# Performance work log

Measured on AMD Instinct MI355X. Metric: run time of the kernel, lower is better.

Reference implementation:

```python
import jax, jax.numpy as jnp
import numpy as np

NEG_INF = jnp.float32(-1e30)  # stand-in for -inf; relu(-inf) == relu(-1e30) == 0


def setup_inputs() -> dict:
    key = jax.random.key(0)
    ks = jax.random.split(key, 8)
    B, S, E = 4, 4096, 512
    query = jax.random.normal(ks[0], (B, S, E), dtype=jnp.float32)
    k_in = jax.random.normal(ks[1], (B, S, E), dtype=jnp.float32)
    v_in = jax.random.normal(ks[2], (B, S, E), dtype=jnp.float32)
    mask = jax.random.randint(ks[3], (B, S, S), 0, 2) > 0  # bool [B,S,S]
    scale = 1.0 / np.sqrt(E)
    W1 = jax.random.uniform(ks[4], (E, E), jnp.float32, -scale, scale)
    b1 = jax.random.uniform(ks[5], (E,), jnp.float32, -scale, scale)
    W2 = jax.random.uniform(ks[6], (E, E), jnp.float32, -scale, scale)
    b2 = jax.random.uniform(ks[7], (E,), jnp.float32, -scale, scale)
    return {"query": query, "key": k_in, "value": v_in, "mask": mask,
            "W1": W1, "b1": b1, "W2": W2, "b2": b2}


def reference(query, key, value, mask, W1, b1, W2, b2):
    # key projection: nn.Linear -> x @ W.T + b
    k = jnp.einsum('bse,fe->bsf', key, W1) + b1
    # raw dot-product correlation scores [B, S, S]
    scores = jnp.einsum('bqe,bke->bqk', query, k)
    # module forces mask[:, :, 0] = True, then fills ~mask with -inf
    m = mask.at[:, :, 0].set(True)
    scores = jnp.where(m, scores, NEG_INF)
    # ReLU instead of softmax (no normalization); dropout is identity in eval
    alpha = jax.nn.relu(scores)
    # value projection then AV matmul
    v = jnp.einsum('bse,fe->bsf', value, W2) + b2
    out = jnp.einsum('bqk,bke->bqe', alpha, v)
    return out
```

## Files before the change

kernel.cpp:

```cpp
#include <hip/hip_runtime.h>
#include <cstdint>


typedef __bf16 bf16x8 __attribute__((ext_vector_type(8)));
typedef float f32x4 __attribute__((ext_vector_type(4)));

__device__ __forceinline__ unsigned short f2bf(float f) {
  unsigned int u = __float_as_uint(f);
  u += 0x7fffu + ((u >> 16) & 1u);
  return (unsigned short)(u >> 16);
}

__device__ __forceinline__ void async_load16(const void* g, void* l) {
  __builtin_amdgcn_global_load_lds(
      (const __attribute__((address_space(1))) unsigned int*)(uintptr_t)g,
      (__attribute__((address_space(3))) unsigned int*)(unsigned int)(uintptr_t)l,
      16, 0, 0);
}

__global__ void __launch_bounds__(256)
prep(const float* __restrict__ q, const float* __restrict__ k,
     const float* __restrict__ v, const float* __restrict__ w1,
     const float* __restrict__ w2, const int* __restrict__ m,
     unsigned short* __restrict__ qb, unsigned short* __restrict__ kb,
     unsigned short* __restrict__ vb, unsigned short* __restrict__ w1b,
     unsigned short* __restrict__ w2b, unsigned int* __restrict__ bits) {
  const int b = blockIdx.x, tid = threadIdx.x;
  if (b < 24576) {
    const int which = b >> 13;
    const int idx = (b & 8191) * 256 + tid;
    const float* in = (which == 0) ? q : (which == 1) ? k : v;
    unsigned short* out = (which == 0) ? qb : (which == 1) ? kb : vb;
    float4 f = ((const float4*)in)[idx];
    ushort4 o;
    o.x = f2bf(f.x); o.y = f2bf(f.y); o.z = f2bf(f.z); o.w = f2bf(f.w);
    ((ushort4*)out)[idx] = o;
  } else if (b < 25088) {
    const int which = (b - 24576) >> 8;
    const int idx = ((b - 24576) & 255) * 256 + tid;
    const float* in = (which == 0) ? w1 : w2;
    unsigned short* out = (which == 0) ? w1b : w2b;
    float4 f = ((const float4*)in)[idx];
    ushort4 o;
    o.x = f2bf(f.x); o.y = f2bf(f.y); o.z = f2bf(f.z); o.w = f2bf(f.w);
    ((ushort4*)out)[idx] = o;
  } else {
    const int lane = tid & 63;
    const size_t wid = (size_t)(b - 25088) * 4 + (tid >> 6);
    const size_t base = wid * 256;
    unsigned long long bl[4];
#pragma unroll
    for (int c = 0; c < 4; ++c) {
      size_t e = base + (size_t)c * 64 + lane;
      int col = (int)(e & 4095);
      bl[c] = __ballot((m[e] != 0) || (col == 0));
    }
    if (lane < 8)
      bits[base / 32 + lane] = (unsigned int)(bl[lane >> 1] >> ((lane & 1) * 32));
  }
}

__global__ void __launch_bounds__(256)
proj(const unsigned short* __restrict__ Kb, const unsigned short* __restrict__ W1b,
     unsigned short* __restrict__ Kp, const float* __restrict__ b1,
     const unsigned short* __restrict__ W2b, const unsigned short* __restrict__ Vb,
     unsigned short* __restrict__ Vpt, const float* __restrict__ b2) {
  constexpr int K = 512;
  constexpr long long SE = 4096LL * 512;
  __shared__ unsigned short sA[2 * 128 * 32];
  __shared__ unsigned short sB[2 * 128 * 32];

  const int L = blockIdx.x;
  const unsigned short *Ab, *Bb;
  unsigned short* C;
  const float* bias;
  int tm0, tn0, N, epi;
  if (L < 512) {
    tn0 = (L & 3) * 128; tm0 = (L >> 2) * 128;
    Ab = Kb; Bb = W1b; C = Kp; bias = b1; N = 512; epi = 0;
  } else {
    const int t = L - 512;
    tn0 = (t & 31) * 128; tm0 = ((t >> 5) & 3) * 128;
    const int bz = t >> 7;
    Ab = W2b; Bb = Vb + (size_t)bz * SE; C = Vpt + (size_t)bz * SE;
    bias = b2; N = 4096; epi = 1;
  }

  const int tid = threadIdx.x;
  const int lane = tid & 63, wave = tid >> 6;
  const int ldrow = lane >> 2, lcol = (lane & 3) * 8;
  const int wm = (wave >> 1) * 64, wn = (wave & 1) * 64;
  const int lr = lane & 15, lq = lane >> 4;

  f32x4 acc[4][4] = {};

  for (int k0 = 0; k0 < K; k0 += 64) {
#pragma unroll
    for (int g = 0; g < 2; ++g)
#pragma unroll
      for (int l = 0; l < 2; ++l) {
        const int row = wave * 32 + l * 16;
        async_load16(Ab + (size_t)(tm0 + row + ldrow) * K + (k0 + g * 32 + lcol),
                     &sA[g * 4096 + row * 32]);
        async_load16(Bb + (size_t)(tn0 + row + ldrow) * K + (k0 + g * 32 + lcol),
                     &sB[g * 4096 + row * 32]);
      }
    __syncthreads();
#pragma unroll
    for (int g = 0; g < 2; ++g) {
      bf16x8 af[4], bfr[4];
#pragma unroll
      for (int t = 0; t < 4; ++t) {
        af[t]  = *(const bf16x8*)&sA[g * 4096 + (wm + t * 16 + lr) * 32 + lq * 8];
        bfr[t] = *(const bf16x8*)&sB[g * 4096 + (wn + t * 16 + lr) * 32 + lq * 8];
      }
#pragma unroll
      for (int mt = 0; mt < 4; ++mt)
#pragma unroll
        for (int nt = 0; nt < 4; ++nt)
          acc[mt][nt] = __builtin_amdgcn_mfma_f32_16x16x32_bf16(af[mt], bfr[nt],
                                                                acc[mt][nt], 0, 0, 0);
    }
    __syncthreads();
  }

#pragma unroll
  for (int mt = 0; mt < 4; ++mt)
#pragma unroll
    for (int r = 0; r < 4; ++r) {
      const int mm = tm0 + wm + mt * 16 + lq * 4 + r;
#pragma unroll
      for (int nt = 0; nt < 4; ++nt) {
        const int n = tn0 + wn + nt * 16 + lr;
        float v = acc[mt][nt][r];
        v += (epi == 0) ? bias[n] : bias[mm];
        C[(size_t)mm * N + n] = f2bf(v);
      }
    }
}

template <int EPI>
__global__ void __launch_bounds__(256)
gemm_bt(const unsigned short* __restrict__ A, const unsigned short* __restrict__ B,
        void* __restrict__ Cout, const unsigned int* __restrict__ mbits,
        int M, int N, int K,
        long long strA, long long strB, long long strC, long long strM) {
  __shared__ unsigned short sA[2 * 128 * 32];
  __shared__ unsigned short sB[2 * 128 * 32];

  const int tid  = threadIdx.x;
  const int lane = tid & 63;
  const int wave = tid >> 6;
  const int bz   = blockIdx.z;
  const int tn0  = blockIdx.x * 128;
  const int tm0  = blockIdx.y * 128;

  const unsigned short* Ab = A + (size_t)bz * strA;
  const unsigned short* Bb = B + (size_t)bz * strB;

  const int ldrow = lane >> 2;
  const int lcol  = (lane & 3) * 8;
  const int wm = (wave >> 1) * 64;
  const int wn = (wave & 1) * 64;
  const int lr = lane & 15;
  const int lq = lane >> 4;

  f32x4 acc[4][4] = {};

  for (int k0 = 0; k0 < K; k0 += 64) {
#pragma unroll
    for (int g = 0; g < 2; ++g)
#pragma unroll
      for (int l = 0; l < 2; ++l) {
        const int row = wave * 32 + l * 16;
        async_load16(Ab + (size_t)(tm0 + row + ldrow) * K + (k0 + g * 32 + lcol),
                     &sA[g * 4096 + row * 32]);
        async_load16(Bb + (size_t)(tn0 + row + ldrow) * K + (k0 + g * 32 + lcol),
                     &sB[g * 4096 + row * 32]);
      }
    __syncthreads();
#pragma unroll
    for (int g = 0; g < 2; ++g) {
      bf16x8 af[4], bfr[4];
#pragma unroll
      for (int t = 0; t < 4; ++t) {
        af[t]  = *(const bf16x8*)&sA[g * 4096 + (wm + t * 16 + lr) * 32 + lq * 8];
        bfr[t] = *(const bf16x8*)&sB[g * 4096 + (wn + t * 16 + lr) * 32 + lq * 8];
      }
#pragma unroll
      for (int mt = 0; mt < 4; ++mt)
#pragma unroll
        for (int nt = 0; nt < 4; ++nt)
          acc[mt][nt] = __builtin_amdgcn_mfma_f32_16x16x32_bf16(af[mt], bfr[nt],
                                                                acc[mt][nt], 0, 0, 0);
    }
    __syncthreads();
  }

#pragma unroll
  for (int mt = 0; mt < 4; ++mt) {
#pragma unroll
    for (int r = 0; r < 4; ++r) {
      const int m = tm0 + wm + mt * 16 + lq * 4 + r;
      unsigned long long w64 = 0;
      if constexpr (EPI == 2) {
        w64 = *(const unsigned long long*)&mbits[(size_t)bz * strM +
                                                 (size_t)m * (N >> 5) + ((tn0 + wn) >> 5)];
      }
#pragma unroll
      for (int nt = 0; nt < 4; ++nt) {
        const int n = tn0 + wn + nt * 16 + lr;
        float v = acc[mt][nt][r];
        if constexpr (EPI == 2) {
          v = ((w64 >> (nt * 16 + lr)) & 1ull) ? fmaxf(v, 0.f) : 0.f;
          ((unsigned short*)Cout)[(size_t)bz * strC + (size_t)m * N + n] = f2bf(v);
        } else {
          ((float*)Cout)[(size_t)bz * strC + (size_t)m * N + n] = v;
        }
      }
    }
  }
}

extern "C" void kernel_launch(void* const* d_in, const int* in_sizes, int n_in,
                              void* d_out, int out_size, void* d_ws, size_t ws_size,
                              hipStream_t stream) {
  const float* query = (const float*)d_in[0];
  const float* key   = (const float*)d_in[1];
  const float* value = (const float*)d_in[2];
  const int*   mask  = (const int*)d_in[3];
  const float* W1    = (const float*)d_in[4];
  const float* b1    = (const float*)d_in[5];
  const float* W2    = (const float*)d_in[6];
  const float* b2    = (const float*)d_in[7];
  float* out = (float*)d_out;

  constexpr int B = 4, S = 4096, E = 512;
  constexpr long long BSE = (long long)B * S * E;
  constexpr long long SE  = (long long)S * E;
  constexpr long long SS  = (long long)S * S;
  constexpr long long BSS = (long long)B * S * S;
  constexpr long long EE  = (long long)E * E;

  char* ws = (char*)d_ws;
  unsigned short* Qb   = (unsigned short*)ws;  ws += BSE * 2;
  unsigned short* Kb   = (unsigned short*)ws;  ws += BSE * 2;
  unsigned short* Vb   = (unsigned short*)ws;  ws += BSE * 2;
  unsigned short* W1b  = (unsigned short*)ws;  ws += EE * 2;
  unsigned short* W2b  = (unsigned short*)ws;  ws += EE * 2;
  unsigned short* Kp   = (unsigned short*)ws;  ws += BSE * 2;
  unsigned short* Vpt  = (unsigned short*)ws;  ws += BSE * 2;
  unsigned short* alph = (unsigned short*)ws;  ws += BSS * 2;
  unsigned int*   mbit = (unsigned int*)ws;    ws += BSS / 8;

  prep<<<dim3(24576 + 512 + 65536), 256, 0, stream>>>(
      query, key, value, W1, W2, mask, Qb, Kb, Vb, W1b, W2b, mbit);

  proj<<<dim3(1024), 256, 0, stream>>>(Kb, W1b, Kp, b1, W2b, Vb, Vpt, b2);

  gemm_bt<2><<<dim3(S / 128, S / 128, B), 256, 0, stream>>>(
      Qb, Kp, alph, mbit, S, S, E, SE, SE, SS, SS / 32);

  gemm_bt<3><<<dim3(E / 128, S / 128, B), 256, 0, stream>>>(
      alph, Vpt, out, nullptr, S, E, S, SS, SE, SE, 0);
}
```

Baseline: 698.8 us.

## Add 256x256 tiled pipelined GEMM kernel for masked QK^T scores

Adds a new 512-thread GEMM kernel with 256x256 output tiles, a K-step of 64 with double-buffered LDS, an XOR-swizzled shared layout, interleaved async global-to-LDS staging between MFMA quarters, s_setprio around MFMA blocks, and a remapped block index for L2 locality. It replaces the 128x128 kernel for the masked ReLU score GEMM to raise data reuse per tile and overlap loads with compute. The old kernel drops its masked epilogue because it now serves only the AV GEMM. Larger tiles mean more register pressure and fewer blocks, which may limit occupancy.

```diff
diff --git a/kernel.cpp b/kernel.cpp
--- a/kernel.cpp
+++ b/kernel.cpp
@@ -140,6 +140,170 @@
 }
 
 template <int EPI>
+__global__ void __launch_bounds__(512, 2)
+gemm256(const unsigned short* __restrict__ A, const unsigned short* __restrict__ B,
+        void* __restrict__ Cout, const unsigned int* __restrict__ mbits,
+        int M, int N, int K,
+        long long strA, long long strB, long long strC, long long strM) {
+  __shared__ unsigned short sA[2][256][64];
+  __shared__ unsigned short sB[2][256][64];
+
+  int lin = blockIdx.x;
+  lin = (lin & 7) * ((int)gridDim.x >> 3) + (lin >> 3);
+  const int tilesN = N >> 8;
+  const int tilesM = M >> 8;
+  const int bx = lin % tilesN;
+  const int by = (lin / tilesN) % tilesM;
+  const int bz = lin / (tilesN * tilesM);
+
+  const int tn0 = bx << 8, tm0 = by << 8;
+  const unsigned short* Ab = A + (size_t)bz * strA;
+  const unsigned short* Bb = B + (size_t)bz * strB;
+
+  const int tid  = threadIdx.x;
+  const int lane = tid & 63;
+  const int w    = tid >> 6;
+  const int wr   = w >> 2;
+  const int wc   = w & 3;
+  const int lr   = lane & 15;
+  const int lq   = lane >> 4;
+
+  const int srow = tid >> 3;
+  const int scol = (((tid & 7) ^ (srow & 7)) << 3);
+  const int sdst = tid << 4;
+
+#define STAGE64(bufbase, g, t0, k0, R0)                                      \
+  async_load16((g) + (size_t)((t0) + (R0) + srow) * K + (k0) + scol,         \
+               (char*)(bufbase) + ((R0) << 7) + sdst)
+
+  const int sxor  = (lr & 7) << 4;
+  const int k0off = (lq << 4) ^ sxor;
+  const int k1off = (64 | (lq << 4)) ^ sxor;
+  const int aRow  = (wr * 128 + lr) * 128;
+  const int bRow  = (wc * 64 + lr) * 128;
+
+#define LDA(d, mh, mt2, kk)                                                  \
+  (*(const bf16x8*)((const char*)sA[d] + aRow + (mh) * 8192 + (mt2) * 2048 + \
+                    k##kk##off))
+#define LDB(d, nh, nt2, kk)                                                  \
+  (*(const bf16x8*)((const char*)sB[d] + bRow + (nh) * 4096 + (nt2) * 2048 + \
+                    k##kk##off))
+
+  f32x4 acc[8][4] = {};
+  bf16x8 afr[4][2];
+  bf16x8 bfr[4][2];
+
+#define RDA(d, mh)                                                           \
+  _Pragma("unroll") for (int mt2 = 0; mt2 < 4; ++mt2) {                      \
+    afr[mt2][0] = LDA(d, mh, mt2, 0);                                        \
+    afr[mt2][1] = LDA(d, mh, mt2, 1);                                        \
+  }
+#define RDB(d, nh)                                                           \
+  _Pragma("unroll") for (int nt2 = 0; nt2 < 2; ++nt2) {                      \
+    bfr[(nh) * 2 + nt2][0] = LDB(d, nh, nt2, 0);                             \
+    bfr[(nh) * 2 + nt2][1] = LDB(d, nh, nt2, 1);                             \
+  }
+#define MFMAQ(mh, nh)                                                        \
+  __builtin_amdgcn_s_setprio(1);                                             \
+  _Pragma("unroll") for (int mt2 = 0; mt2 < 4; ++mt2)                        \
+  _Pragma("unroll") for (int nt2 = 0; nt2 < 2; ++nt2) {                      \
+    acc[(mh) * 4 + mt2][(nh) * 2 + nt2] =                                    \
+        __builtin_amdgcn_mfma_f32_16x16x32_bf16(                             \
+            afr[mt2][0], bfr[(nh) * 2 + nt2][0],                             \
+            acc[(mh) * 4 + mt2][(nh) * 2 + nt2], 0, 0, 0);                   \
+    acc[(mh) * 4 + mt2][(nh) * 2 + nt2] =                                    \
+        __builtin_amdgcn_mfma_f32_16x16x32_bf16(                             \
+            afr[mt2][1], bfr[(nh) * 2 + nt2][1],                             \
+            acc[(mh) * 4 + mt2][(nh) * 2 + nt2], 0, 0, 0);                   \
+  }                                                                          \
+  __builtin_amdgcn_s_setprio(0);
+#define BAR __builtin_amdgcn_s_barrier()
+
+  const int nIter = K >> 7;
+
+  STAGE64(sB[0], Bb, tn0, 0, 0);   STAGE64(sB[0], Bb, tn0, 0, 64);
+  STAGE64(sB[0], Bb, tn0, 0, 128); STAGE64(sB[0], Bb, tn0, 0, 192);
+  STAGE64(sA[0], Ab, tm0, 0, 0);   STAGE64(sA[0], Ab, tm0, 0, 64);
+  STAGE64(sA[0], Ab, tm0, 0, 128); STAGE64(sA[0], Ab, tm0, 0, 192);
+  STAGE64(sB[1], Bb, tn0, 64, 0);  STAGE64(sB[1], Bb, tn0, 64, 64);
+  STAGE64(sB[1], Bb, tn0, 64, 128);STAGE64(sB[1], Bb, tn0, 64, 192);
+  asm volatile("s_waitcnt vmcnt(4)" ::: "memory");
+  BAR;
+
+  for (int j = 0; j < nIter; ++j) {
+    const int kb = j << 7;
+    const bool pf = (j + 1 < nIter);
+    RDA(0, 0); RDB(0, 0);
+    STAGE64(sA[1], Ab, tm0, kb + 64, 0);
+    STAGE64(sA[1], Ab, tm0, kb + 64, 64);
+    BAR; MFMAQ(0, 0); BAR;
+    RDB(0, 1);
+    STAGE64(sA[1], Ab, tm0, kb + 64, 128);
+    STAGE64(sA[1], Ab, tm0, kb + 64, 192);
+    BAR; MFMAQ(0, 1); BAR;
+    RDA(0, 1);
+    if (pf) { STAGE64(sB[0], Bb, tn0, kb + 128, 0);
+              STAGE64(sB[0], Bb, tn0, kb + 128, 64); }
+    BAR; MFMAQ(1, 1); BAR;
+    if (pf) { STAGE64(sB[0], Bb, tn0, kb + 128, 128);
+              STAGE64(sB[0], Bb, tn0, kb + 128, 192); }
+    BAR; MFMAQ(1, 0);
+    if (pf) asm volatile("s_waitcnt vmcnt(4)" ::: "memory");
+    else    asm volatile("s_waitcnt vmcnt(0)" ::: "memory");
+    BAR;
+    RDA(1, 0); RDB(1, 0);
+    if (pf) { STAGE64(sA[0], Ab, tm0, kb + 128, 0);
+              STAGE64(sA[0], Ab, tm0, kb + 128, 64); }
+    BAR; MFMAQ(0, 0); BAR;
+    RDB(1, 1);
+    if (pf) { STAGE64(sA[0], Ab, tm0, kb + 128, 128);
+              STAGE64(sA[0], Ab, tm0, kb + 128, 192); }
+    BAR; MFMAQ(0, 1); BAR;
+    RDA(1, 1);
+    if (pf) { STAGE64(sB[1], Bb, tn0, kb + 192, 0);
+              STAGE64(sB[1], Bb, tn0, kb + 192, 64); }
+    BAR; MFMAQ(1, 1); BAR;
+    if (pf) { STAGE64(sB[1], Bb, tn0, kb + 192, 128);
+              STAGE64(sB[1], Bb, tn0, kb + 192, 192); }
+    BAR; MFMAQ(1, 0);
+    asm volatile("s_waitcnt vmcnt(4)" ::: "memory");
+    BAR;
+  }
+
+#pragma unroll
+  for (int mt = 0; mt < 8; ++mt) {
+#pragma unroll
+    for (int r = 0; r < 4; ++r) {
+      const int m = tm0 + wr * 128 + mt * 16 + lq * 4 + r;
+      unsigned long long w64 = 0;
+      if constexpr (EPI == 2) {
+        w64 = *(const unsigned long long*)&mbits[(size_t)bz * strM +
+                                                 (size_t)m * (N >> 5) +
+                                                 ((tn0 + wc * 64) >> 5)];
+      }
+#pragma unroll
+      for (int nt = 0; nt < 4; ++nt) {
+        const int n = tn0 + wc * 64 + nt * 16 + lr;
+        float v = acc[mt][nt][r];
+        if constexpr (EPI == 2) {
+          v = ((w64 >> (nt * 16 + lr)) & 1ull) ? fmaxf(v, 0.f) : 0.f;
+          ((unsigned short*)Cout)[(size_t)bz * strC + (size_t)m * N + n] = f2bf(v);
+        } else {
+          ((float*)Cout)[(size_t)bz * strC + (size_t)m * N + n] = v;
+        }
+      }
+    }
+  }
+#undef STAGE64
+#undef LDA
+#undef LDB
+#undef RDA
+#undef RDB
+#undef MFMAQ
+#undef BAR
+}
+
+template <int EPI>
 __global__ void __launch_bounds__(256)
 gemm_bt(const unsigned short* __restrict__ A, const unsigned short* __restrict__ B,
         void* __restrict__ Cout, const unsigned int* __restrict__ mbits,
@@ -202,21 +366,11 @@
 #pragma unroll
     for (int r = 0; r < 4; ++r) {
       const int m = tm0 + wm + mt * 16 + lq * 4 + r;
-      unsigned long long w64 = 0;
-      if constexpr (EPI == 2) {
-        w64 = *(const unsigned long long*)&mbits[(size_t)bz * strM +
-                                                 (size_t)m * (N >> 5) + ((tn0 + wn) >> 5)];
-      }
 #pragma unroll
       for (int nt = 0; nt < 4; ++nt) {
         const int n = tn0 + wn + nt * 16 + lr;
         float v = acc[mt][nt][r];
-        if constexpr (EPI == 2) {
-          v = ((w64 >> (nt * 16 + lr)) & 1ull) ? fmaxf(v, 0.f) : 0.f;
-          ((unsigned short*)Cout)[(size_t)bz * strC + (size_t)m * N + n] = f2bf(v);
-        } else {
-          ((float*)Cout)[(size_t)bz * strC + (size_t)m * N + n] = v;
-        }
+        ((float*)Cout)[(size_t)bz * strC + (size_t)m * N + n] = v;
       }
     }
   }
@@ -258,7 +412,7 @@
 
   proj<<<dim3(1024), 256, 0, stream>>>(Kb, W1b, Kp, b1, W2b, Vb, Vpt, b2);
 
-  gemm_bt<2><<<dim3(S / 128, S / 128, B), 256, 0, stream>>>(
+  gemm256<2><<<dim3((S / 256) * (S / 256) * B), 512, 0, stream>>>(
       Qb, Kp, alph, mbit, S, S, E, SE, SE, SS, SS / 32);
 
   gemm_bt<3><<<dim3(E / 128, S / 128, B), 256, 0, stream>>>(
```

New measurement: 662.6 us. -5.2%, faster.

## Fuse QK^T mask-relu and AV matmuls into one flash-style kernel

Applied to the files above, without the earlier changes.

Replaces the two separate GEMM launches (scores to a bf16 [B,S,S] buffer, then alpha@V) with one fused kernel. Each block handles 64 query rows for the full E=512 output and streams K and V tiles through LDS. The masked ReLU scores are written to a small swizzled LDS tile and consumed immediately. This removes the 128 MB intermediate alpha write and read, but it launches only 256 blocks of 512 threads and uses large LDS and register footprints, so occupancy and parallelism drop.

```diff
diff --git a/kernel.cpp b/kernel.cpp
--- a/kernel.cpp
+++ b/kernel.cpp
@@ -139,87 +139,133 @@
     }
 }
 
-template <int EPI>
-__global__ void __launch_bounds__(256)
-gemm_bt(const unsigned short* __restrict__ A, const unsigned short* __restrict__ B,
-        void* __restrict__ Cout, const unsigned int* __restrict__ mbits,
-        int M, int N, int K,
-        long long strA, long long strB, long long strC, long long strM) {
-  __shared__ unsigned short sA[2 * 128 * 32];
-  __shared__ unsigned short sB[2 * 128 * 32];
+__global__ void __launch_bounds__(512, 2)
+fused_av(const unsigned short* __restrict__ Qb,
+         const unsigned short* __restrict__ Kp,
+         const unsigned short* __restrict__ Vpt,
+         const unsigned long long* __restrict__ mb,
+         float* __restrict__ out) {
+  constexpr int S = 4096, E = 512;
+  __shared__ unsigned short sK[64 * 512];
+  __shared__ unsigned short sV[512 * 64];
+  __shared__ unsigned short sP[64 * 64];
+
+  int lin = blockIdx.x;
+  lin = (lin & 7) * 32 + (lin >> 3);
+  const int bz = lin >> 6;
+  const int qbase = (lin & 63) << 6;
 
   const int tid  = threadIdx.x;
   const int lane = tid & 63;
-  const int wave = tid >> 6;
-  const int bz   = blockIdx.z;
-  const int tn0  = blockIdx.x * 128;
-  const int tm0  = blockIdx.y * 128;
-
-  const unsigned short* Ab = A + (size_t)bz * strA;
-  const unsigned short* Bb = B + (size_t)bz * strB;
-
-  const int ldrow = lane >> 2;
-  const int lcol  = (lane & 3) * 8;
-  const int wm = (wave >> 1) * 64;
-  const int wn = (wave & 1) * 64;
-  const int lr = lane & 15;
-  const int lq = lane >> 4;
+  const int w    = tid >> 6;
+  const int lr   = lane & 15;
+  const int lq   = lane >> 4;
+  const int mi   = w >> 1;
+  const int np   = w & 1;
+
+  const unsigned short* Kpb = Kp  + (size_t)bz * S * E;
+  const unsigned short* Vpb = Vpt + (size_t)bz * E * S;
+  const unsigned short* Qp  = Qb  + ((size_t)bz * S + qbase) * E;
+
+  const int rK   = tid >> 6;
+  const int cK   = ((tid & 63) ^ rK) << 3;
+  const int srow = tid >> 3;
+  const int scol = (((tid & 7) ^ (srow & 7)) << 3);
+  const int sdst = tid << 4;
+
+#define STG_K(kt)                                                            \
+  _Pragma("unroll") for (int R0 = 0; R0 < 64; R0 += 8)                       \
+      async_load16(Kpb + (size_t)((kt) * 64 + R0 + rK) * E + cK,             \
+                   (char*)sK + R0 * 1024 + sdst);
+#define STG_V(kt)                                                            \
+  _Pragma("unroll") for (int R0 = 0; R0 < 512; R0 += 64)                     \
+      async_load16(Vpb + (size_t)(R0 + srow) * S + (kt) * 64 + scol,         \
+                   (char*)sV + R0 * 128 + sdst);
+
+  STG_K(0);
+  bf16x8 qreg[16];
+#pragma unroll
+  for (int s = 0; s < 16; ++s)
+    qreg[s] = *(const bf16x8*)(Qp + (size_t)(mi * 16 + lr) * E + s * 32 + lq * 8);
 
   f32x4 acc[4][4] = {};
-
-  for (int k0 = 0; k0 < K; k0 += 64) {
-#pragma unroll
-    for (int g = 0; g < 2; ++g)
-#pragma unroll
-      for (int l = 0; l < 2; ++l) {
-        const int row = wave * 32 + l * 16;
-        async_load16(Ab + (size_t)(tm0 + row + ldrow) * K + (k0 + g * 32 + lcol),
-                     &sA[g * 4096 + row * 32]);
-        async_load16(Bb + (size_t)(tn0 + row + ldrow) * K + (k0 + g * 32 + lcol),
-                     &sB[g * 4096 + row * 32]);
-      }
-    __syncthreads();
-#pragma unroll
-    for (int g = 0; g < 2; ++g) {
-      bf16x8 af[4], bfr[4];
-#pragma unroll
-      for (int t = 0; t < 4; ++t) {
-        af[t]  = *(const bf16x8*)&sA[g * 4096 + (wm + t * 16 + lr) * 32 + lq * 8];
-        bfr[t] = *(const bf16x8*)&sB[g * 4096 + (wn + t * 16 + lr) * 32 + lq * 8];
-      }
-#pragma unroll
-      for (int mt = 0; mt < 4; ++mt)
-#pragma unroll
-        for (int nt = 0; nt < 4; ++nt)
-          acc[mt][nt] = __builtin_amdgcn_mfma_f32_16x16x32_bf16(af[mt], bfr[nt],
-                                                                acc[mt][nt], 0, 0, 0);
-    }
-    __syncthreads();
+  const int swz = (lr & 7) << 4;
+
+  for (int kt = 0; kt < 64; ++kt) {
+    asm volatile("s_waitcnt vmcnt(0)" ::: "memory");
+    __builtin_amdgcn_s_barrier();
+    STG_V(kt);
+    unsigned long long wmk[4];
+#pragma unroll
+    for (int r = 0; r < 4; ++r)
+      wmk[r] = mb[((size_t)bz * S + qbase + mi * 16 + lq * 4 + r) * 64 + kt];
+
+    f32x4 sa0 = {0.f, 0.f, 0.f, 0.f}, sa1 = {0.f, 0.f, 0.f, 0.f};
+    __builtin_amdgcn_s_setprio(1);
+#pragma unroll
+    for (int s = 0; s < 16; ++s) {
+      const int cb = (s * 64 + lq * 16) ^ swz;
+      bf16x8 b0 = *(const bf16x8*)((const char*)sK + (np * 32 + lr) * 1024 + cb);
+      bf16x8 b1 = *(const bf16x8*)((const char*)sK + (np * 32 + 16 + lr) * 1024 + cb);
+      sa0 = __builtin_amdgcn_mfma_f32_16x16x32_bf16(qreg[s], b0, sa0, 0, 0, 0);
+      sa1 = __builtin_amdgcn_mfma_f32_16x16x32_bf16(qreg[s], b1, sa1, 0, 0, 0);
+    }
+    __builtin_amdgcn_s_setprio(0);
+
+#pragma unroll
+    for (int r = 0; r < 4; ++r) {
+      const int q = mi * 16 + lq * 4 + r;
+      const int rowb = q * 128;
+      const int qswz = (q & 7) << 4;
+      {
+        const int k = (np * 2) * 16 + lr;
+        float v = sa0[r];
+        v = ((wmk[r] >> k) & 1ull) ? fmaxf(v, 0.f) : 0.f;
+        *(unsigned short*)((char*)sP + rowb + ((2 * k) ^ qswz)) = f2bf(v);
+      }
+      {
+        const int k = (np * 2 + 1) * 16 + lr;
+        float v = sa1[r];
+        v = ((wmk[r] >> k) & 1ull) ? fmaxf(v, 0.f) : 0.f;
+        *(unsigned short*)((char*)sP + rowb + ((2 * k) ^ qswz)) = f2bf(v);
+      }
+    }
+    asm volatile("s_waitcnt vmcnt(0) lgkmcnt(0)" ::: "memory");
+    __builtin_amdgcn_s_barrier();
+    if (kt < 63) STG_K(kt + 1);
+    __builtin_amdgcn_s_setprio(1);
+#pragma unroll
+    for (int ks = 0; ks < 2; ++ks) {
+      const int cb = (ks * 64 + lq * 16) ^ swz;
+      bf16x8 pa[4], vb[4];
+#pragma unroll
+      for (int m2 = 0; m2 < 4; ++m2)
+        pa[m2] = *(const bf16x8*)((const char*)sP + (m2 * 16 + lr) * 128 + cb);
+#pragma unroll
+      for (int n2 = 0; n2 < 4; ++n2)
+        vb[n2] = *(const bf16x8*)((const char*)sV + (w * 64 + n2 * 16 + lr) * 128 + cb);
+#pragma unroll
+      for (int m2 = 0; m2 < 4; ++m2)
+#pragma unroll
+        for (int n2 = 0; n2 < 4; ++n2)
+          acc[m2][n2] = __builtin_amdgcn_mfma_f32_16x16x32_bf16(
+              pa[m2], vb[n2], acc[m2][n2], 0, 0, 0);
+    }
+    __builtin_amdgcn_s_setprio(0);
   }
 
-#pragma unroll
-  for (int mt = 0; mt < 4; ++mt) {
+  float* outp = out + ((size_t)bz * S + qbase) * E + w * 64;
+#pragma unroll
+  for (int m2 = 0; m2 < 4; ++m2)
 #pragma unroll
     for (int r = 0; r < 4; ++r) {
-      const int m = tm0 + wm + mt * 16 + lq * 4 + r;
-      unsigned long long w64 = 0;
-      if constexpr (EPI == 2) {
-        w64 = *(const unsigned long long*)&mbits[(size_t)bz * strM +
-                                                 (size_t)m * (N >> 5) + ((tn0 + wn) >> 5)];
-      }
-#pragma unroll
-      for (int nt = 0; nt < 4; ++nt) {
-        const int n = tn0 + wn + nt * 16 + lr;
-        float v = acc[mt][nt][r];
-        if constexpr (EPI == 2) {
-          v = ((w64 >> (nt * 16 + lr)) & 1ull) ? fmaxf(v, 0.f) : 0.f;
-          ((unsigned short*)Cout)[(size_t)bz * strC + (size_t)m * N + n] = f2bf(v);
-        } else {
-          ((float*)Cout)[(size_t)bz * strC + (size_t)m * N + n] = v;
-        }
-      }
-    }
-  }
+      const size_t rowo = (size_t)(m2 * 16 + lq * 4 + r) * E;
+#pragma unroll
+      for (int n2 = 0; n2 < 4; ++n2)
+        outp[rowo + n2 * 16 + lr] = acc[m2][n2][r];
+    }
+#undef STG_K
+#undef STG_V
 }
 
 extern "C" void kernel_launch(void* const* d_in, const int* in_sizes, int n_in,
@@ -237,8 +283,6 @@
 
   constexpr int B = 4, S = 4096, E = 512;
   constexpr long long BSE = (long long)B * S * E;
-  constexpr long long SE  = (long long)S * E;
-  constexpr long long SS  = (long long)S * S;
   constexpr long long BSS = (long long)B * S * S;
   constexpr long long EE  = (long long)E * E;
 
@@ -250,7 +294,6 @@
   unsigned short* W2b  = (unsigned short*)ws;  ws += EE * 2;
   unsigned short* Kp   = (unsigned short*)ws;  ws += BSE * 2;
   unsigned short* Vpt  = (unsigned short*)ws;  ws += BSE * 2;
-  unsigned short* alph = (unsigned short*)ws;  ws += BSS * 2;
   unsigned int*   mbit = (unsigned int*)ws;    ws += BSS / 8;
 
   prep<<<dim3(24576 + 512 + 65536), 256, 0, stream>>>(
@@ -258,9 +301,6 @@
 
   proj<<<dim3(1024), 256, 0, stream>>>(Kb, W1b, Kp, b1, W2b, Vb, Vpt, b2);
 
-  gemm_bt<2><<<dim3(S / 128, S / 128, B), 256, 0, stream>>>(
-      Qb, Kp, alph, mbit, S, S, E, SE, SE, SS, SS / 32);
-
-  gemm_bt<3><<<dim3(E / 128, S / 128, B), 256, 0, stream>>>(
-      alph, Vpt, out, nullptr, S, E, S, SS, SE, SE, 0);
-}
+  fused_av<<<dim3(256), 512, 0, stream>>>(
+      Qb, Kp, Vpt, (const unsigned long long*)mbit, out);
+}
```

Result: faster. 649.9 us (-7.0%).
